# Optimization experiments

Hardware: AMD Instinct MI355X
Metric: run time of the kernel (lower is better)

## Reference

```python
import jax, jax.numpy as jnp
import numpy as np

IN_F, HID, OUT_F = 171, 1024, 171

def _cond_lst(condition_num, groundtruth_num, seq_len):
    num_cycles = seq_len // (condition_num + groundtruth_num) + 1
    lst = np.zeros((num_cycles, condition_num + groundtruth_num), dtype=np.float32)
    lst[:, :groundtruth_num] = 1.0
    return lst.reshape(-1)[:seq_len]

def setup_inputs() -> dict:
    key = jax.random.key(0)
    ks = jax.random.split(key, 16)
    s = 0.02
    inp = {
        'real_seq': jax.random.normal(ks[0], (128, 128, IN_F), jnp.float32),
        'W_ih1': jax.random.normal(ks[1], (4 * HID, IN_F), jnp.float32) * s,
        'W_hh1': jax.random.normal(ks[2], (4 * HID, HID), jnp.float32) * s,
        'b_ih1': jnp.zeros((4 * HID,), jnp.float32),
        'b_hh1': jnp.zeros((4 * HID,), jnp.float32),
        'W_ih2': jax.random.normal(ks[3], (4 * HID, HID), jnp.float32) * s,
        'W_hh2': jax.random.normal(ks[4], (4 * HID, HID), jnp.float32) * s,
        'b_ih2': jnp.zeros((4 * HID,), jnp.float32),
        'b_hh2': jnp.zeros((4 * HID,), jnp.float32),
        'W_ih3': jax.random.normal(ks[5], (4 * HID, HID), jnp.float32) * s,
        'W_hh3': jax.random.normal(ks[6], (4 * HID, HID), jnp.float32) * s,
        'b_ih3': jnp.zeros((4 * HID,), jnp.float32),
        'b_hh3': jnp.zeros((4 * HID,), jnp.float32),
        'W_dec': jax.random.normal(ks[7], (OUT_F, HID), jnp.float32) * s,
        'b_dec': jnp.zeros((OUT_F,), jnp.float32),
        'condition_num': 5,
        'groundtruth_num': 5,
    }
    return inp

def _lstm_cell(x, h, c, Wih, Whh, bih, bhh):
    # PyTorch LSTMCell: gates ordered i, f, g, o
    g = x @ Wih.T + bih + h @ Whh.T + bhh
    i, f, gg, o = jnp.split(g, 4, axis=-1)
    c2 = jax.nn.sigmoid(f) * c + jax.nn.sigmoid(i) * jnp.tanh(gg)
    h2 = jax.nn.sigmoid(o) * jnp.tanh(c2)
    return h2, c2

def reference(real_seq, W_ih1, W_hh1, b_ih1, b_hh1, W_ih2, W_hh2, b_ih2, b_hh2,
              W_ih3, W_hh3, b_ih3, b_hh3, W_dec, b_dec, condition_num, groundtruth_num):
    B, T, _ = real_seq.shape
    cond = jnp.asarray(_cond_lst(condition_num, groundtruth_num, T))  # [T], 1=use ground truth
    z = jnp.zeros((B, HID), jnp.float32)
    carry0 = (z, z, z, z, z, z, jnp.zeros((B, OUT_F), jnp.float32))
    xs = (jnp.swapaxes(real_seq, 0, 1), cond)  # time-major

    def step(carry, x):
        h0, h1, h2, c0, c1, c2, out_frame = carry
        frame, c_flag = x
        in_frame = jnp.where(c_flag > 0.5, frame, out_frame)
        h0, c0 = _lstm_cell(in_frame, h0, c0, W_ih1, W_hh1, b_ih1, b_hh1)
        h1, c1 = _lstm_cell(h0, h1, c1, W_ih2, W_hh2, b_ih2, b_hh2)
        h2, c2 = _lstm_cell(h1, h2, c2, W_ih3, W_hh3, b_ih3, b_hh3)
        out_frame = h2 @ W_dec.T + b_dec
        return (h0, h1, h2, c0, c1, c2, out_frame), out_frame

    _, out_seq = jax.lax.scan(step, carry0, xs)  # [T, B, OUT_F]
    return jnp.swapaxes(out_seq, 0, 1)  # [B, T, OUT_F]
```

## Files before the change

kernel.cpp:

```cpp
#include <hip/hip_runtime.h>

#define TT 128
#define INF 171

typedef _Float16 half8 __attribute__((ext_vector_type(8)));
typedef float floatx4 __attribute__((ext_vector_type(4)));
typedef unsigned short u16;

#define XBSZ 163840
#define HSZ  131072

#define WAITV(n) asm volatile("s_waitcnt vmcnt(" #n ")" ::: "memory")
#define SCHEDB() __builtin_amdgcn_sched_barrier(0)

__device__ __forceinline__ u16 f2h(float f){
  _Float16 h = (_Float16)f;
  return __builtin_bit_cast(u16, h);
}
__device__ __forceinline__ float sigm(float x){ return 1.f/(1.f+__expf(-x)); }
__device__ __forceinline__ float tanh_(float x){ return 1.f - 2.f/(__expf(2.f*x)+1.f); }

__device__ __forceinline__ void scat_coh(u16* buf, int nch, int b, int k, u16 v){
  u16* p = buf + (size_t)((((b>>4)*nch + (k>>5))*4 + ((k>>3)&3))*16 + (b&15))*8 + (k&7);
  unsigned int vv = v;
  asm volatile("global_store_short %0, %1, off sc0 sc1" :: "v"(p), "v"(vv) : "memory");
}
__device__ __forceinline__ void ld16_coh(half8& d, const u16* p){
  asm volatile("global_load_dwordx4 %0, %1, off sc0 sc1" : "=&v"(d) : "v"(p) : "memory");
}

template<int NB>
__device__ __forceinline__ void issue_pair(const u16* s0, const u16* s1,
    half8* v, int tid, int beat0){
  #pragma unroll
  for (int i=0;i<NB;i++) ld16_coh(v[i],    s0 + (size_t)(beat0+i)*4096 + (size_t)tid*8);
  #pragma unroll
  for (int i=0;i<NB;i++) ld16_coh(v[NB+i], s1 + (size_t)(beat0+i)*4096 + (size_t)tid*8);
}

__global__ __launch_bounds__(256) void prep_w1f(const float* __restrict__ Wih1,
    const float* __restrict__ Whh1, u16* __restrict__ Wf){
  int u = blockIdx.x*256 + threadIdx.x;
  int tile = u / 2560;
  int r = u - tile*2560;
  int kc = r >> 6, l = r & 63;
  int row = (tile>>6)*1024 + (tile&63)*16 + (l&15);
  int k0 = kc*32 + ((l>>4)<<3);
  half8 hv;
  #pragma unroll
  for (int e=0;e<8;e++){
    int k = k0+e;
    float w = 0.f;
    if (k < 171)       w = Wih1[(size_t)row*171 + k];
    else if (k < 1195) w = Whh1[(size_t)row*1024 + (k-171)];
    hv[e] = (_Float16)w;
  }
  *(half8*)&Wf[(size_t)(tile*40 + kc)*512 + (size_t)l*8] = hv;
}

__global__ __launch_bounds__(256) void prep_w23f(const float* __restrict__ Wih2,
    const float* __restrict__ Whh2, const float* __restrict__ Wih3,
    const float* __restrict__ Whh3, u16* __restrict__ W2f, u16* __restrict__ W3f){
  int u = blockIdx.x*256 + threadIdx.x;
  int tile = u >> 12;
  int r = u & 4095;
  int kc = r >> 6, l = r & 63;
  int row = (tile>>6)*1024 + (tile&63)*16 + (l&15);
  int k0 = kc*32 + ((l>>4)<<3);
  half8 h2, h3;
  #pragma unroll
  for (int e=0;e<8;e++){
    int k = k0+e;
    size_t si = (size_t)row*1024 + (k & 1023);
    h2[e] = (_Float16)((k < 1024) ? Wih2[si] : Whh2[si]);
    h3[e] = (_Float16)((k < 1024) ? Wih3[si] : Whh3[si]);
  }
  size_t base = (size_t)(tile*64 + kc)*512 + (size_t)l*8;
  *(half8*)&W2f[base] = h2;
  *(half8*)&W3f[base] = h3;
}

__global__ __launch_bounds__(256) void prep_wdecf(const float* __restrict__ Wdec,
    u16* __restrict__ Wdf){
  int u = blockIdx.x*256 + threadIdx.x;
  int tile = u / 2048;
  int r = u & 2047;
  int kc = r >> 6, l = r & 63;
  int row = tile*16 + (l&15);
  int k0 = kc*32 + ((l>>4)<<3);
  half8 hv;
  #pragma unroll
  for (int e=0;e<8;e++){
    int k = k0+e;
    hv[e] = (_Float16)((row < 171) ? Wdec[(size_t)row*1024 + k] : 0.f);
  }
  *(half8*)&Wdf[(size_t)(tile*32 + kc)*512 + (size_t)l*8] = hv;
}

__global__ __launch_bounds__(256) void prep_misc(
    const float* __restrict__ rseq, const int* __restrict__ gnp,
    const float* __restrict__ bih1, const float* __restrict__ bhh1,
    const float* __restrict__ bih2, const float* __restrict__ bhh2,
    const float* __restrict__ bih3, const float* __restrict__ bhh3,
    const float* __restrict__ bdec,
    u16* __restrict__ Xb1f, u16* __restrict__ Hf, float* __restrict__ cbuf,
    float* __restrict__ b1, float* __restrict__ b2, float* __restrict__ b3,
    float* __restrict__ bd, int* __restrict__ bar)
{
  size_t idx = (size_t)blockIdx.x*256 + threadIdx.x;
  if (idx < 327680){
    int q = (int)(idx / 163840);
    int rem = (int)(idx % 163840);
    int btile = rem / 20480;
    int r2 = rem % 20480;
    int kc = r2 >> 9, r3 = r2 & 511;
    int l = r3 >> 3, e = r3 & 7;
    int b = btile*16 + (l&15);
    int k = kc*32 + ((l>>4)<<3) + e;
    float v = 0.f;
    if (q==0 && k < 171 && *gnp > 0) v = rseq[(size_t)b*TT*INF + k];
    Xb1f[idx] = f2h(v);
    return;
  }
  idx -= 327680;
  if (idx < 786432){ Hf[idx] = 0; return; }
  idx -= 786432;
  if (idx < 393216){ cbuf[idx] = 0.f; return; }
  idx -= 393216;
  if (idx < 12288){
    int which = (int)(idx >> 12), j = (int)(idx & 4095);
    float v = (which==0)? (bih1[j]+bhh1[j]) : (which==1)? (bih2[j]+bhh2[j]) : (bih3[j]+bhh3[j]);
    ((which==0)?b1:(which==1)?b2:b3)[j] = v;
    return;
  }
  idx -= 12288;
  if (idx < 176){ bd[idx] = (idx < 171) ? bdec[idx] : 0.f; return; }
  idx -= 176;
  if (idx < 512) bar[idx] = 0;
}

__device__ __forceinline__ void gridbar(int* __restrict__ bar, int cls, int hv,
                                        int bc, int* s_dead){
  __syncthreads();
  if (threadIdx.x == 0 && !(*s_dead)){
    int* arr = &bar[cls*64 + hv*32];
    int* gen = &bar[256 + cls*32];
    bool released = false;
    int o = __hip_atomic_fetch_add(arr, 1, __ATOMIC_RELAXED, __HIP_MEMORY_SCOPE_AGENT);
    if ((o & 31) == 31){
      int og = __hip_atomic_fetch_add(gen, 1, __ATOMIC_RELAXED, __HIP_MEMORY_SCOPE_AGENT);
      released = (og & 1) == 1;
    }
    if (!released){
      long long t0 = clock64();
      while (__hip_atomic_load(gen, __ATOMIC_RELAXED, __HIP_MEMORY_SCOPE_AGENT) < 2*(bc+1)){
        __builtin_amdgcn_s_sleep(2);
        if (clock64() - t0 > 30000000LL){ *s_dead = 1; break; }
      }
    }
  }
  __syncthreads();
}

template<int KHALF, int GS>
__device__ __forceinline__ void gemm_stream(const u16* __restrict__ wp,
    const u16* __restrict__ x0, const u16* __restrict__ x1,
    floatx4& a0, floatx4& a1)
{
  constexpr int NG = KHALF/GS;
  half8 W[2][GS];
  #pragma unroll
  for (int i=0;i<GS;i++)
    W[0][i] = *(const half8*)(wp + (size_t)i*512);
  #pragma unroll
  for (int g8=0; g8<NG; g8++){
    const int cur = g8 & 1, nxt = cur ^ 1;
    if (g8+1 < NG){
      const size_t off = (size_t)(g8+1)*GS*512;
      #pragma unroll
      for (int i=0;i<GS;i++)
        W[nxt][i] = *(const half8*)(wp + off + (size_t)i*512);
    }
    #pragma unroll
    for (int i=0;i<GS;i++){
      half8 xv0 = *(const half8*)(x0 + (size_t)(g8*GS+i)*512);
      half8 xv1 = *(const half8*)(x1 + (size_t)(g8*GS+i)*512);
      a0 = __builtin_amdgcn_mfma_f32_16x16x32_f16(W[cur][i], xv0, a0, 0,0,0);
      a1 = __builtin_amdgcn_mfma_f32_16x16x32_f16(W[cur][i], xv1, a1, 0,0,0);
    }
  }
}

__device__ __forceinline__ void gemm32_llc(const u16* __restrict__ wp,
    const u16* __restrict__ x0, const u16* __restrict__ x1,
    floatx4& a0, floatx4& a1)
{
  half8 W[2][4];
  #pragma unroll
  for (int i=0;i<4;i++) ld16_coh(W[0][i], wp + (size_t)i*512);
  #pragma unroll
  for (int g8=0; g8<8; g8++){
    const int cur = g8 & 1, nxt = cur ^ 1;
    if (g8+1 < 8){
      const size_t off = (size_t)(g8+1)*4*512;
      #pragma unroll
      for (int i=0;i<4;i++) ld16_coh(W[nxt][i], wp + off + (size_t)i*512);
      WAITV(4);
    } else {
      WAITV(0);
    }
    SCHEDB();
    #pragma unroll
    for (int i=0;i<4;i++){
      half8 xv0 = *(const half8*)(x0 + (size_t)(g8*4+i)*512);
      half8 xv1 = *(const half8*)(x1 + (size_t)(g8*4+i)*512);
      a0 = __builtin_amdgcn_mfma_f32_16x16x32_f16(W[cur][i], xv0, a0, 0,0,0);
      a1 = __builtin_amdgcn_mfma_f32_16x16x32_f16(W[cur][i], xv1, a1, 0,0,0);
    }
  }
}

__global__ void __launch_bounds__(512,2) acro_persist(
    const u16* __restrict__ W1f, const u16* __restrict__ W2f,
    const u16* __restrict__ W3f, const u16* __restrict__ Wdf,
    u16* __restrict__ Xb1f, u16* __restrict__ Hf,
    const float* __restrict__ b1, const float* __restrict__ b2,
    const float* __restrict__ b3, const float* __restrict__ bd,
    const float* __restrict__ rseq, float* __restrict__ out,
    const int* __restrict__ cnp, const int* __restrict__ gnp, int* __restrict__ bar)
{
  __shared__ u16 XL[65536];
  __shared__ float gb[8][16][33];
  __shared__ int s_dead;
  const int bId = (int)blockIdx.x;
  const int js = (bId & 7)*8 + ((bId >> 5) & 7);
  const int nq = (bId >> 3) & 3;
  const int bh = (bId >> 5) & 1;
  const int tid = (int)threadIdx.x;
  const int w = tid >> 6, l = tid & 63;
  const int g = w >> 1, hf = w & 1;
  const int l15 = l & 15, lq = l >> 4;
  const int uu = tid >> 5, bq = tid & 31;
  const int jj = js*16 + uu, bgg = nq*32 + bq;
  if (tid == 0) s_dead = 0;
  const int gnv = *gnp;
  int P = *cnp + gnv; if (P < 1) P = 1;
  int bc = 0;

  u16* H0[2] = { Hf,          Hf + HSZ   };
  u16* H1[2] = { Hf + 2*HSZ,  Hf + 3*HSZ };
  u16* H2[2] = { Hf + 4*HSZ,  Hf + 5*HSZ };

  float bs1[4], bs2[4], bs3[4];
  #pragma unroll
  for (int q=0;q<4;q++){
    bs1[q] = b1[q*1024 + jj];
    bs2[q] = b2[q*1024 + jj];
    bs3[q] = b3[q*1024 + jj];
  }
  const bool dec_act = (js < 11);
  const int oo = js*16 + uu;
  const float bdr = dec_act ? bd[oo] : 0.f;
  float c0r = 0.f, c1r = 0.f, c2r = 0.f;

  half8 pf1[8], pf2[8], pf3[8];
  issue_pair<4>(Xb1f + (size_t)(nq*2  )*20480,
                Xb1f + (size_t)(nq*2+1)*20480, pf1, tid, 1);

  __syncthreads();
  for (int t=0; t<TT; t++){
    const int pr = t & 1, nx = pr ^ 1;

    {
      const u16* xb = Xb1f + (size_t)pr*XBSZ;
      half8 fr0, fr1;
      ld16_coh(fr0, xb + (size_t)(nq*2  )*20480 + (size_t)tid*8);
      ld16_coh(fr1, xb + (size_t)(nq*2+1)*20480 + (size_t)tid*8);
      WAITV(0);
      SCHEDB();
      *(half8*)&XL[(size_t)tid*8] = fr0;
      *(half8*)&XL[(size_t)5*4096 + (size_t)tid*8] = fr1;
      #pragma unroll
      for (int i=0;i<4;i++){
        *(half8*)&XL[(size_t)(1+i)*4096 + (size_t)tid*8] = pf1[i];
        *(half8*)&XL[(size_t)(6+i)*4096 + (size_t)tid*8] = pf1[4+i];
      }
      __syncthreads();
      const u16* wp = W1f + ((size_t)(g*64 + js)*40 + (size_t)hf*20)*512 + (size_t)(l<<3);
      const u16* x0 = XL + (size_t)hf*10240 + (size_t)(l<<3);
      const u16* x1 = x0 + 20480;
      floatx4 a0{}, a1{};
      gemm_stream<20,4>(wp, x0, x1, a0, a1);
      #pragma unroll
      for (int r=0;r<4;r++){
        gb[w][lq*4+r][l15]      = a0[r];
        gb[w][lq*4+r][16 + l15] = a1[r];
      }
      __syncthreads();
      {
        float gi = gb[0][uu][bq] + gb[1][uu][bq] + bs1[0];
        float gf = gb[2][uu][bq] + gb[3][uu][bq] + bs1[1];
        float gg = gb[4][uu][bq] + gb[5][uu][bq] + bs1[2];
        float go = gb[6][uu][bq] + gb[7][uu][bq] + bs1[3];
        float c = sigm(gf)*c0r + sigm(gi)*tanh_(gg);
        c0r = c;
        u16 hb = f2h(sigm(go)*tanh_(c));
        scat_coh(H0[pr], 32, bgg, jj, hb);
        scat_coh(Xb1f + (size_t)nx*XBSZ, 40, bgg, 171 + jj, hb);
      }
      issue_pair<4>(H1[nx] + (size_t)(nq*2  )*16384,
                    H1[nx] + (size_t)(nq*2+1)*16384, pf2, tid, 0);
    }
    WAITV(8);
    gridbar(bar, nq, bh, bc, &s_dead); bc++;

    {
      half8 fr[8];
      issue_pair<4>(H0[pr] + (size_t)(nq*2  )*16384,
                    H0[pr] + (size_t)(nq*2+1)*16384, fr, tid, 0);
      WAITV(0);
      SCHEDB();
      #pragma unroll
      for (int i=0;i<8;i++) *(half8*)&XL[(size_t)i*4096 + (size_t)tid*8] = fr[i];
      #pragma unroll
      for (int i=0;i<8;i++) *(half8*)&XL[32768 + (size_t)i*4096 + (size_t)tid*8] = pf2[i];
      __syncthreads();
      const u16* wp = W2f + ((size_t)(g*64 + js)*64 + (size_t)hf*32)*512 + (size_t)(l<<3);
      const u16* x0 = XL + (size_t)hf*32768 + (size_t)(l<<3);
      const u16* x1 = x0 + 16384;
      floatx4 a0{}, a1{};
      gemm_stream<32,8>(wp, x0, x1, a0, a1);
      #pragma unroll
      for (int r=0;r<4;r++){
        gb[w][lq*4+r][l15]      = a0[r];
        gb[w][lq*4+r][16 + l15] = a1[r];
      }
      __syncthreads();
      {
        float gi = gb[0][uu][bq] + gb[1][uu][bq] + bs2[0];
        float gf = gb[2][uu][bq] + gb[3][uu][bq] + bs2[1];
        float gg = gb[4][uu][bq] + gb[5][uu][bq] + bs2[2];
        float go = gb[6][uu][bq] + gb[7][uu][bq] + bs2[3];
        float c = sigm(gf)*c1r + sigm(gi)*tanh_(gg);
        c1r = c;
        u16 hb = f2h(sigm(go)*tanh_(c));
        scat_coh(H1[pr], 32, bgg, jj, hb);
      }
      issue_pair<4>(H2[nx] + (size_t)(nq*2  )*16384,
                    H2[nx] + (size_t)(nq*2+1)*16384, pf3, tid, 0);
    }
    WAITV(8);
    gridbar(bar, nq, bh, bc, &s_dead); bc++;

    {
      half8 fr[8];
      issue_pair<4>(H1[pr] + (size_t)(nq*2  )*16384,
                    H1[pr] + (size_t)(nq*2+1)*16384, fr, tid, 0);
      WAITV(0);
      SCHEDB();
      #pragma unroll
      for (int i=0;i<8;i++) *(half8*)&XL[(size_t)i*4096 + (size_t)tid*8] = fr[i];
      #pragma unroll
      for (int i=0;i<8;i++) *(half8*)&XL[32768 + (size_t)i*4096 + (size_t)tid*8] = pf3[i];
      __syncthreads();
      const u16* wp = W3f + ((size_t)(g*64 + js)*64 + (size_t)hf*32)*512 + (size_t)(l<<3);
      const u16* x0 = XL + (size_t)hf*32768 + (size_t)(l<<3);
      const u16* x1 = x0 + 16384;
      floatx4 a0{}, a1{};
      gemm32_llc(wp, x0, x1, a0, a1);
      #pragma unroll
      for (int r=0;r<4;r++){
        gb[w][lq*4+r][l15]      = a0[r];
        gb[w][lq*4+r][16 + l15] = a1[r];
      }
      __syncthreads();
      {
        float gi = gb[0][uu][bq] + gb[1][uu][bq] + bs3[0];
        float gf = gb[2][uu][bq] + gb[3][uu][bq] + bs3[1];
        float gg = gb[4][uu][bq] + gb[5][uu][bq] + bs3[2];
        float go = gb[6][uu][bq] + gb[7][uu][bq] + bs3[3];
        float c = sigm(gf)*c2r + sigm(gi)*tanh_(gg);
        c2r = c;
        u16 hb = f2h(sigm(go)*tanh_(c));
        scat_coh(H2[pr], 32, bgg, jj, hb);
      }
    }
    WAITV(0);
    gridbar(bar, nq, bh, bc, &s_dead); bc++;

    if (dec_act){
      half8 fd[8];
      issue_pair<4>(H2[pr] + (size_t)(nq*2  )*16384,
                    H2[pr] + (size_t)(nq*2+1)*16384, fd, tid, 0);
      WAITV(0);
      SCHEDB();
      #pragma unroll
      for (int i=0;i<8;i++) *(half8*)&XL[(size_t)i*4096 + (size_t)tid*8] = fd[i];
      __syncthreads();
      const u16* wp = Wdf + (size_t)(js*32 + w*4)*512 + (size_t)(l<<3);
      const u16* x0 = XL + (size_t)(w*4)*512 + (size_t)(l<<3);
      const u16* x1 = x0 + 16384;
      floatx4 d0{}, d1{};
      #pragma unroll
      for (int i=0;i<4;i++){
        half8 wv  = *(const half8*)(wp + (size_t)i*512);
        half8 a0v = *(const half8*)(x0 + (size_t)i*512);
        half8 a1v = *(const half8*)(x1 + (size_t)i*512);
        d0 = __builtin_amdgcn_mfma_f32_16x16x32_f16(wv, a0v, d0, 0,0,0);
        d1 = __builtin_amdgcn_mfma_f32_16x16x32_f16(wv, a1v, d1, 0,0,0);
      }
      #pragma unroll
      for (int r=0;r<4;r++){
        gb[w][lq*4+r][l15]      = d0[r];
        gb[w][lq*4+r][16 + l15] = d1[r];
      }
      __syncthreads();
      const int nf = (((t+1) % P) < gnv) ? 1 : 0;
      if (oo < 171){
        float v = bdr;
        #pragma unroll
        for (int i=0;i<8;i++) v += gb[i][uu][bq];
        out[((size_t)bgg*TT + t)*INF + oo] = v;
        if (t+1 < TT){
          float src = nf ? rseq[((size_t)bgg*TT + (t+1))*INF + oo] : v;
          scat_coh(Xb1f + (size_t)nx*XBSZ, 40, bgg, oo, f2h(src));
        }
      }
    }
    if (t+1 < TT){
      const u16* xbn = Xb1f + (size_t)nx*XBSZ;
      issue_pair<4>(xbn + (size_t)(nq*2  )*20480,
                    xbn + (size_t)(nq*2+1)*20480, pf1, tid, 1);
      WAITV(8);
    } else {
      WAITV(0);
    }
    gridbar(bar, nq, bh, bc, &s_dead); bc++;
  }
}

extern "C" void kernel_launch(void* const* d_in, const int* in_sizes, int n_in,
                              void* d_out, int out_size, void* d_ws, size_t ws_size,
                              hipStream_t stream)
{
  const float* rseq = (const float*)d_in[0];
  const float* Wih1 = (const float*)d_in[1];
  const float* Whh1 = (const float*)d_in[2];
  const float* bih1 = (const float*)d_in[3];
  const float* bhh1 = (const float*)d_in[4];
  const float* Wih2 = (const float*)d_in[5];
  const float* Whh2 = (const float*)d_in[6];
  const float* bih2 = (const float*)d_in[7];
  const float* bhh2 = (const float*)d_in[8];
  const float* Wih3 = (const float*)d_in[9];
  const float* Whh3 = (const float*)d_in[10];
  const float* bih3 = (const float*)d_in[11];
  const float* bhh3 = (const float*)d_in[12];
  const float* Wdec = (const float*)d_in[13];
  const float* bdec = (const float*)d_in[14];
  const int* cn = (const int*)d_in[15];
  const int* gn = (const int*)d_in[16];
  float* out = (float*)d_out;

  char* p = (char*)d_ws;
  auto take = [&](size_t n){ void* r = (void*)p; p += (n + 255) & ~(size_t)255; return r; };
  u16* W1f  = (u16*)take(5242880UL*2);
  u16* W2f  = (u16*)take(8388608UL*2);
  u16* W3f  = (u16*)take(8388608UL*2);
  u16* Wdf  = (u16*)take(180224UL*2);
  u16* Xb1f = (u16*)take(327680UL*2);
  u16* Hf   = (u16*)take(786432UL*2);
  float* cbuf = (float*)take(393216UL*4);
  float* b1 = (float*)take(4096*4);
  float* b2 = (float*)take(4096*4);
  float* b3 = (float*)take(4096*4);
  float* bd = (float*)take(176*4);
  int* bar  = (int*)take(512*4);
  if ((size_t)(p - (char*)d_ws) > ws_size) return;

  prep_w1f  <<<2560,256,0,stream>>>(Wih1, Whh1, W1f);
  prep_w23f <<<4096,256,0,stream>>>(Wih2, Whh2, Wih3, Whh3, W2f, W3f);
  prep_wdecf<<<88,  256,0,stream>>>(Wdec, Wdf);
  prep_misc <<<5939,256,0,stream>>>(rseq, gn, bih1,bhh1,bih2,bhh2,bih3,bhh3,bdec,
                                    Xb1f, Hf, cbuf, b1,b2,b3,bd, bar);

  acro_persist<<<256,512,0,stream>>>(W1f, W2f, W3f, Wdf, Xb1f, Hf,
                                     b1, b2, b3, bd, rseq, out, cn, gn, bar);
}
```

Baseline: 4.454 ms.

## Defer decoder off the critical path on teacher-forced steps, saving a grid barrier

When the next step uses ground-truth input, the decoder output for the current step is not needed for the recurrence. Its matvec and output write are postponed into the start of the next iteration, and that step skips one grid-wide barrier. The ground-truth frame is now read straight from real_seq into the layer-1 input tile instead of being scattered into the shared buffer. The next-input prefetch is issued earlier, inside the layer-3 block. In exchange the code is more complex, with three copies of the decoder code, extra strided reads of real_seq per block, and a final drain after the loop.

```diff
diff --git a/kernel.cpp b/kernel.cpp
--- a/kernel.cpp
+++ b/kernel.cpp
@@ -246,6 +246,7 @@
   const int gnv = *gnp;
   int P = *cnp + gnv; if (P < 1) P = 1;
   int bc = 0;
+  int pend = 0, pt = 0;
 
   u16* H0[2] = { Hf,          Hf + HSZ   };
   u16* H1[2] = { Hf + 2*HSZ,  Hf + 3*HSZ };
@@ -261,7 +262,12 @@
   const bool dec_act = (js < 11);
   const int oo = js*16 + uu;
   const float bdr = dec_act ? bd[oo] : 0.f;
+  const u16* wpd = Wdf + (size_t)(js*32 + w*4)*512 + (size_t)(l<<3);
   float c0r = 0.f, c1r = 0.f, c2r = 0.f;
+
+  const int kq0 = (tid>>6)*32 + ((tid&63)>>4)*8;
+  const int pb0 = nq*32 + (tid&15);
+  const int pb1 = pb0 + 16;
 
   half8 pf1[8], pf2[8], pf3[8];
   issue_pair<4>(Xb1f + (size_t)(nq*2  )*20480,
@@ -270,14 +276,71 @@
   __syncthreads();
   for (int t=0; t<TT; t++){
     const int pr = t & 1, nx = pr ^ 1;
+
+    if (pend){
+      if (dec_act){
+        const int pp = pt & 1;
+        half8 fd[8];
+        issue_pair<4>(H2[pp] + (size_t)(nq*2  )*16384,
+                      H2[pp] + (size_t)(nq*2+1)*16384, fd, tid, 0);
+        WAITV(0);
+        SCHEDB();
+        #pragma unroll
+        for (int i=0;i<8;i++) *(half8*)&XL[(size_t)i*4096 + (size_t)tid*8] = fd[i];
+        __syncthreads();
+        const u16* x0 = XL + (size_t)(w*4)*512 + (size_t)(l<<3);
+        const u16* x1 = x0 + 16384;
+        floatx4 d0{}, d1{};
+        #pragma unroll
+        for (int i=0;i<4;i++){
+          half8 wv  = *(const half8*)(wpd + (size_t)i*512);
+          half8 a0v = *(const half8*)(x0 + (size_t)i*512);
+          half8 a1v = *(const half8*)(x1 + (size_t)i*512);
+          d0 = __builtin_amdgcn_mfma_f32_16x16x32_f16(wv, a0v, d0, 0,0,0);
+          d1 = __builtin_amdgcn_mfma_f32_16x16x32_f16(wv, a1v, d1, 0,0,0);
+        }
+        #pragma unroll
+        for (int r=0;r<4;r++){
+          gb[w][lq*4+r][l15]      = d0[r];
+          gb[w][lq*4+r][16 + l15] = d1[r];
+        }
+        __syncthreads();
+        if (oo < 171){
+          float v = bdr;
+          #pragma unroll
+          for (int i=0;i<8;i++) v += gb[i][uu][bq];
+          out[((size_t)bgg*TT + pt)*INF + oo] = v;
+        }
+      }
+      pend = 0;
+    }
 
     {
       const u16* xb = Xb1f + (size_t)pr*XBSZ;
       half8 fr0, fr1;
       ld16_coh(fr0, xb + (size_t)(nq*2  )*20480 + (size_t)tid*8);
       ld16_coh(fr1, xb + (size_t)(nq*2+1)*20480 + (size_t)tid*8);
+      const bool teach = (t > 0) && ((t % P) < gnv);
+      float pv0[8], pv1[8];
+      if (teach && kq0 < 171){
+        #pragma unroll
+        for (int e=0;e<8;e++){
+          int k = kq0 + e;
+          if (k < 171){
+            pv0[e] = rseq[((size_t)pb0*TT + t)*INF + k];
+            pv1[e] = rseq[((size_t)pb1*TT + t)*INF + k];
+          }
+        }
+      }
       WAITV(0);
       SCHEDB();
+      if (teach && kq0 < 171){
+        #pragma unroll
+        for (int e=0;e<8;e++){
+          int k = kq0 + e;
+          if (k < 171){ fr0[e] = (_Float16)pv0[e]; fr1[e] = (_Float16)pv1[e]; }
+        }
+      }
       *(half8*)&XL[(size_t)tid*8] = fr0;
       *(half8*)&XL[(size_t)5*4096 + (size_t)tid*8] = fr1;
       #pragma unroll
@@ -384,58 +447,93 @@
         u16 hb = f2h(sigm(go)*tanh_(c));
         scat_coh(H2[pr], 32, bgg, jj, hb);
       }
-    }
+      if (t+1 < TT){
+        const u16* xbn = Xb1f + (size_t)nx*XBSZ;
+        issue_pair<4>(xbn + (size_t)(nq*2  )*20480,
+                      xbn + (size_t)(nq*2+1)*20480, pf1, tid, 1);
+      }
+    }
+    if (t+1 < TT){ WAITV(8); } else { WAITV(0); }
+    gridbar(bar, nq, bh, bc, &s_dead); bc++;
+
+    {
+      const int nfn = (t+1 < TT) && (((t+1) % P) < gnv);
+      if (nfn || t+1 == TT){
+        pend = 1; pt = t;
+      } else {
+        if (dec_act){
+          half8 fd[8];
+          issue_pair<4>(H2[pr] + (size_t)(nq*2  )*16384,
+                        H2[pr] + (size_t)(nq*2+1)*16384, fd, tid, 0);
+          WAITV(0);
+          SCHEDB();
+          #pragma unroll
+          for (int i=0;i<8;i++) *(half8*)&XL[(size_t)i*4096 + (size_t)tid*8] = fd[i];
+          __syncthreads();
+          const u16* x0 = XL + (size_t)(w*4)*512 + (size_t)(l<<3);
+          const u16* x1 = x0 + 16384;
+          floatx4 d0{}, d1{};
+          #pragma unroll
+          for (int i=0;i<4;i++){
+            half8 wv  = *(const half8*)(wpd + (size_t)i*512);
+            half8 a0v = *(const half8*)(x0 + (size_t)i*512);
+            half8 a1v = *(const half8*)(x1 + (size_t)i*512);
+            d0 = __builtin_amdgcn_mfma_f32_16x16x32_f16(wv, a0v, d0, 0,0,0);
+            d1 = __builtin_amdgcn_mfma_f32_16x16x32_f16(wv, a1v, d1, 0,0,0);
+          }
+          #pragma unroll
+          for (int r=0;r<4;r++){
+            gb[w][lq*4+r][l15]      = d0[r];
+            gb[w][lq*4+r][16 + l15] = d1[r];
+          }
+          __syncthreads();
+          if (oo < 171){
+            float v = bdr;
+            #pragma unroll
+            for (int i=0;i<8;i++) v += gb[i][uu][bq];
+            out[((size_t)bgg*TT + t)*INF + oo] = v;
+            scat_coh(Xb1f + (size_t)nx*XBSZ, 40, bgg, oo, f2h(v));
+          }
+        }
+        WAITV(0);
+        gridbar(bar, nq, bh, bc, &s_dead); bc++;
+      }
+    }
+  }
+
+  if (pend && dec_act){
+    const int pp = pt & 1;
+    half8 fd[8];
+    issue_pair<4>(H2[pp] + (size_t)(nq*2  )*16384,
+                  H2[pp] + (size_t)(nq*2+1)*16384, fd, tid, 0);
     WAITV(0);
-    gridbar(bar, nq, bh, bc, &s_dead); bc++;
-
-    if (dec_act){
-      half8 fd[8];
-      issue_pair<4>(H2[pr] + (size_t)(nq*2  )*16384,
-                    H2[pr] + (size_t)(nq*2+1)*16384, fd, tid, 0);
-      WAITV(0);
-      SCHEDB();
-      #pragma unroll
-      for (int i=0;i<8;i++) *(half8*)&XL[(size_t)i*4096 + (size_t)tid*8] = fd[i];
-      __syncthreads();
-      const u16* wp = Wdf + (size_t)(js*32 + w*4)*512 + (size_t)(l<<3);
-      const u16* x0 = XL + (size_t)(w*4)*512 + (size_t)(l<<3);
-      const u16* x1 = x0 + 16384;
-      floatx4 d0{}, d1{};
-      #pragma unroll
-      for (int i=0;i<4;i++){
-        half8 wv  = *(const half8*)(wp + (size_t)i*512);
-        half8 a0v = *(const half8*)(x0 + (size_t)i*512);
-        half8 a1v = *(const half8*)(x1 + (size_t)i*512);
-        d0 = __builtin_amdgcn_mfma_f32_16x16x32_f16(wv, a0v, d0, 0,0,0);
-        d1 = __builtin_amdgcn_mfma_f32_16x16x32_f16(wv, a1v, d1, 0,0,0);
-      }
-      #pragma unroll
-      for (int r=0;r<4;r++){
-        gb[w][lq*4+r][l15]      = d0[r];
-        gb[w][lq*4+r][16 + l15] = d1[r];
-      }
-      __syncthreads();
-      const int nf = (((t+1) % P) < gnv) ? 1 : 0;
-      if (oo < 171){
-        float v = bdr;
-        #pragma unroll
-        for (int i=0;i<8;i++) v += gb[i][uu][bq];
-        out[((size_t)bgg*TT + t)*INF + oo] = v;
-        if (t+1 < TT){
-          float src = nf ? rseq[((size_t)bgg*TT + (t+1))*INF + oo] : v;
-          scat_coh(Xb1f + (size_t)nx*XBSZ, 40, bgg, oo, f2h(src));
-        }
-      }
-    }
-    if (t+1 < TT){
-      const u16* xbn = Xb1f + (size_t)nx*XBSZ;
-      issue_pair<4>(xbn + (size_t)(nq*2  )*20480,
-                    xbn + (size_t)(nq*2+1)*20480, pf1, tid, 1);
-      WAITV(8);
-    } else {
-      WAITV(0);
-    }
-    gridbar(bar, nq, bh, bc, &s_dead); bc++;
+    SCHEDB();
+    #pragma unroll
+    for (int i=0;i<8;i++) *(half8*)&XL[(size_t)i*4096 + (size_t)tid*8] = fd[i];
+    __syncthreads();
+    const u16* x0 = XL + (size_t)(w*4)*512 + (size_t)(l<<3);
+    const u16* x1 = x0 + 16384;
+    floatx4 d0{}, d1{};
+    #pragma unroll
+    for (int i=0;i<4;i++){
+      half8 wv  = *(const half8*)(wpd + (size_t)i*512);
+      half8 a0v = *(const half8*)(x0 + (size_t)i*512);
+      half8 a1v = *(const half8*)(x1 + (size_t)i*512);
+      d0 = __builtin_amdgcn_mfma_f32_16x16x32_f16(wv, a0v, d0, 0,0,0);
+      d1 = __builtin_amdgcn_mfma_f32_16x16x32_f16(wv, a1v, d1, 0,0,0);
+    }
+    #pragma unroll
+    for (int r=0;r<4;r++){
+      gb[w][lq*4+r][l15]      = d0[r];
+      gb[w][lq*4+r][16 + l15] = d1[r];
+    }
+    __syncthreads();
+    if (oo < 171){
+      float v = bdr;
+      #pragma unroll
+      for (int i=0;i<8;i++) v += gb[i][uu][bq];
+      out[((size_t)bgg*TT + pt)*INF + oo] = v;
+    }
   }
 }
 
```

New measurement: 4.575 ms. +2.7%, slower.
